# Performance work log

Hardware: AMD Instinct MI355X
Metric: run time of the kernel (lower is better)

## Reference

```python
import jax, jax.numpy as jnp
import numpy as np

HID = 512
POOL = 4096
NUM_OBJ = 151
NUM_REL = 51
K = 100
GROUPS = 8
EPS_GN = 1e-5


def _lrga(x, w, b):
    # LowRankAttention: x [N,D] -> [N,2K]
    tmp = jax.nn.relu(x @ w + b)            # [N,4K]
    u, v, z, t = tmp[:, :K], tmp[:, K:2*K], tmp[:, 2*K:3*K], tmp[:, 3*K:]
    # joint_normalize2: scalar 1 / (mean_n(U @ (V^T 1)) + eps)
    norm = u @ jnp.sum(v, axis=0)           # [N]
    d = 1.0 / (jnp.sum(norm) / x.shape[0] + 1e-6)
    res = u @ (v.T @ z)                     # [N,K], low-rank global attention
    return jax.nn.relu(jnp.concatenate((res * d, t), axis=1))


def _group_norm(x, gamma, beta):
    n, c = x.shape
    xg = x.reshape(n, GROUPS, c // GROUPS)
    mu = jnp.mean(xg, axis=-1, keepdims=True)
    var = jnp.var(xg, axis=-1, keepdims=True)
    xn = ((xg - mu) * jax.lax.rsqrt(var + EPS_GN)).reshape(n, c)
    return xn * gamma + beta


def setup_inputs() -> dict:
    key = jax.random.key(0)
    ks = jax.random.split(key, 24)
    n_obj, n_rel = 4096, 16384
    s = 0.02
    inp = {
        'edge_ctx': jax.random.normal(ks[0], (n_obj, HID), jnp.float32),
        'union_features': jax.random.normal(ks[1], (n_rel, POOL), jnp.float32),
        'rel_pair_idxs': jax.random.randint(ks[2], (n_rel, 2), 0, n_obj),
        'obj_preds': jax.random.randint(ks[3], (n_obj,), 0, NUM_OBJ),
        # parameters
        'w_post_emb': jax.random.normal(ks[4], (HID, 2 * HID), jnp.float32) * s,
        'b_post_emb': jnp.zeros((2 * HID,), jnp.float32),
        'w_post_cat': jax.random.normal(ks[5], (2 * HID, POOL), jnp.float32) * s,
        'b_post_cat': jnp.zeros((POOL,), jnp.float32),
        'w_attn1': jax.random.normal(ks[6], (POOL, 4 * K), jnp.float32) * s,
        'b_attn1': jnp.zeros((4 * K,), jnp.float32),
        'w_dr1': jax.random.normal(ks[7], (2 * K + POOL, POOL), jnp.float32) * s,
        'b_dr1': jnp.zeros((POOL,), jnp.float32),
        'gn_gamma': jnp.ones((POOL,), jnp.float32),
        'gn_beta': jnp.zeros((POOL,), jnp.float32),
        'w_attn2': jax.random.normal(ks[8], (POOL, 4 * K), jnp.float32) * s,
        'b_attn2': jnp.zeros((4 * K,), jnp.float32),
        'w_dr2': jax.random.normal(ks[9], (2 * K + POOL, POOL), jnp.float32) * s,
        'b_dr2': jnp.zeros((POOL,), jnp.float32),
        'w_rel': jax.random.normal(ks[10], (POOL, NUM_REL), jnp.float32) * s,
        'b_rel': jnp.zeros((NUM_REL,), jnp.float32),
        'w_ctx': jax.random.normal(ks[11], (2 * HID, NUM_REL), jnp.float32) * s,
        'b_ctx': jnp.zeros((NUM_REL,), jnp.float32),
        'freq_table': jax.random.normal(ks[12], (NUM_OBJ * NUM_OBJ, NUM_REL), jnp.float32) * s,
    }
    return inp


def reference(edge_ctx, union_features, rel_pair_idxs, obj_preds,
              w_post_emb, b_post_emb, w_post_cat, b_post_cat,
              w_attn1, b_attn1, w_dr1, b_dr1, gn_gamma, gn_beta,
              w_attn2, b_attn2, w_dr2, b_dr2,
              w_rel, b_rel, w_ctx, b_ctx, freq_table):
    # post_emb -> split into head/tail halves (view(N,2,H))
    edge_rep = edge_ctx @ w_post_emb + b_post_emb        # [N_obj, 2H]
    head_rep, tail_rep = edge_rep[:, :HID], edge_rep[:, HID:]
    # gather subject/object features per relation pair
    sub, obj = rel_pair_idxs[:, 0], rel_pair_idxs[:, 1]
    prod_rep = jnp.concatenate((head_rep[sub], tail_rep[obj]), axis=-1)  # [N_rel, 2H]
    pair_pred = obj_preds[rel_pair_idxs]                 # [N_rel, 2]
    ctx_gate = prod_rep @ w_post_cat + b_post_cat        # [N_rel, POOL]
    visual_rep = union_features * ctx_gate
    # LRGA block 1
    x_local = jax.nn.relu(visual_rep)                    # dropout = identity (eval)
    x_global = _lrga(union_features, w_attn1, b_attn1)   # [N_rel, 2K]
    x = jnp.concatenate((x_global, x_local), axis=1) @ w_dr1 + b_dr1
    x = _group_norm(jax.nn.relu(x), gn_gamma, gn_beta)
    # LRGA block 2
    x_local = jax.nn.relu(x)
    x_global = _lrga(x, w_attn2, b_attn2)
    visual_rep = jnp.concatenate((x_global, x_local), axis=1) @ w_dr2 + b_dr2
    # fused classification + frequency-bias lookup-add
    rel_dists = visual_rep @ w_rel + b_rel + prod_rep @ w_ctx + b_ctx
    freq = freq_table[pair_pred[:, 0] * NUM_OBJ + pair_pred[:, 1]]
    rel_dists = rel_dists + freq                         # dropout(0.3) = identity (eval)
    return rel_dists
```

## Files before the change

kernel.cpp:

```cpp
#include <hip/hip_runtime.h>

__device__ __forceinline__ short f2bf(float f) {
    unsigned u = __float_as_uint(f);
    unsigned r = (u + 0x7FFFu + ((u >> 16) & 1u)) >> 16;
    return (short)r;
}
__device__ __forceinline__ float bf2f(short s) {
    return __uint_as_float(((unsigned)(unsigned short)s) << 16);
}

typedef short bf16x8 __attribute__((ext_vector_type(8)));
typedef float f32x4  __attribute__((ext_vector_type(4)));

__device__ __forceinline__ void async16(const void* g, void* l) {
    __builtin_amdgcn_global_load_lds(
        (__attribute__((address_space(1))) unsigned int*)(void*)(g),
        (__attribute__((address_space(3))) unsigned int*)(l), 16, 0, 0);
}

template<int MODE>
__global__ __launch_bounds__(256)
void gemm128(const short* __restrict__ A, long lda,
             const short* __restrict__ B,
             const float* __restrict__ bias,
             void* __restrict__ outp, long ldo, int ooff, int nreal,
             const float* __restrict__ gate, short* __restrict__ gate_bf,
             const int* __restrict__ fidx, const float* __restrict__ freq,
             int K)
{
    __shared__ short As[128 * 64];
    __shared__ short Bs[128 * 64];
    const int t = threadIdx.x;
    const int lane = t & 63;
    const int w = t >> 6;
    const long bm = (long)blockIdx.y * 128;
    const long bn = (long)blockIdx.x * 128;

    f32x4 acc[4][4] = {};

    const short* Ab = A + bm * lda;
    const short* Bb = B + bn * (long)K;

    const int wm = (w & 1) * 64, wn = (w >> 1) * 64;
    const int mrow = lane & 15, khi = (lane >> 4) * 8;
    const int swz = mrow & 7;

    for (int k0 = 0; k0 < K; k0 += 64) {
        __syncthreads();
        #pragma unroll
        for (int i = 0; i < 4; ++i) {
            int idx = i * 256 + t;
            int r = idx >> 3, ch = (idx & 7) ^ (r & 7);
            async16(Ab + (long)r * lda + (k0 + ch * 8), &As[idx * 8]);
        }
        #pragma unroll
        for (int i = 0; i < 4; ++i) {
            int idx = i * 256 + t;
            int r = idx >> 3, ch = (idx & 7) ^ (r & 7);
            async16(Bb + (long)r * K + (k0 + ch * 8), &Bs[idx * 8]);
        }
        __syncthreads();

        #pragma unroll
        for (int kk = 0; kk < 64; kk += 32) {
            const int ch = (((kk + khi) >> 3) ^ swz) * 8;
            bf16x8 a[4], b[4];
            #pragma unroll
            for (int im = 0; im < 4; ++im)
                a[im] = *(const bf16x8*)&As[(wm + im * 16 + mrow) * 64 + ch];
            #pragma unroll
            for (int in = 0; in < 4; ++in)
                b[in] = *(const bf16x8*)&Bs[(wn + in * 16 + mrow) * 64 + ch];
            #pragma unroll
            for (int im = 0; im < 4; ++im)
                #pragma unroll
                for (int in = 0; in < 4; ++in)
                    acc[im][in] = __builtin_amdgcn_mfma_f32_16x16x32_bf16(
                        a[im], b[in], acc[im][in], 0, 0, 0);
        }
    }

    const int col = lane & 15, rb = (lane >> 4) * 4;
    #pragma unroll
    for (int in = 0; in < 4; ++in) {
        long n = bn + wn + in * 16 + col;
        if (n >= nreal) continue;
        float bv = bias[n];
        #pragma unroll
        for (int im = 0; im < 4; ++im) {
            #pragma unroll
            for (int r = 0; r < 4; ++r) {
                long m = bm + wm + im * 16 + rb + r;
                float v = acc[im][in][r] + bv;
                if (MODE == 1) v = fmaxf(v, 0.f);
                if (MODE == 2) {
                    float g = gate[m * 4096 + n];
                    gate_bf[m * 4096 + n] = f2bf(g);
                    v = fmaxf(v * g, 0.f);
                }
                if (MODE == 3) {
                    v += freq[(long)fidx[m] * 51 + n];
                    ((float*)outp)[m * 51 + n] = v;
                } else {
                    ((short*)outp)[m * ldo + ooff + n] = f2bf(v);
                }
            }
        }
    }
}

__global__ void cvt_bf16(const float* __restrict__ in, short* __restrict__ out, long n) {
    long i = (long)blockIdx.x * 256 + threadIdx.x;
    if (i < n) out[i] = f2bf(in[i]);
}

__global__ __launch_bounds__(256)
void transpose_pad(const float* __restrict__ in, int R, int C,
                   short* __restrict__ out, int Cp, int Rp)
{
    __shared__ float tile[32][33];
    int tx = threadIdx.x, ty = threadIdx.y;
    int c0 = blockIdx.x * 32, r0 = blockIdx.y * 32;
    #pragma unroll
    for (int j = 0; j < 32; j += 8) {
        int r = r0 + ty + j, c = c0 + tx;
        tile[ty + j][tx] = (r < R && c < C) ? in[(long)r * C + c] : 0.f;
    }
    __syncthreads();
    #pragma unroll
    for (int j = 0; j < 32; j += 8) {
        int oc = c0 + ty + j;
        int orr = r0 + tx;
        out[(long)oc * Rp + orr] = f2bf(tile[tx][ty + j]);
    }
}

__global__ void build_wf(const float* __restrict__ w_rel, const float* __restrict__ b_rel,
                         const float* __restrict__ w_ctx, const float* __restrict__ b_ctx,
                         short* __restrict__ wf, float* __restrict__ biasF)
{
    long i = (long)blockIdx.x * 256 + threadIdx.x;
    if (i < 64) biasF[i] = (i < 51) ? b_rel[i] + b_ctx[i] : 0.f;
    if (i >= 128L * 5120) return;
    int n = (int)(i / 5120), k = (int)(i % 5120);
    float v = 0.f;
    if (n < 51) v = (k < 4096) ? w_rel[(long)k * 51 + n] : w_ctx[(long)(k - 4096) * 51 + n];
    wf[i] = f2bf(v);
}

__global__ void gather_prod(const short* __restrict__ erep, const int* __restrict__ pairs,
                            const int* __restrict__ obj_preds,
                            short* __restrict__ vrcat, int* __restrict__ fidx)
{
    long i = blockIdx.x;
    int t = threadIdx.x;
    int s = pairs[2 * i], o = pairs[2 * i + 1];
    if (t == 0) fidx[i] = obj_preds[s] * 151 + obj_preds[o];
    int c = t * 4;
    long src = (long)(c < 512 ? s : o) * 1024 + c;
    *(uint2*)(vrcat + i * 5120 + 4096 + c) = *(const uint2*)(erep + src);
}

__global__ void colsum200(const short* __restrict__ tmp, float* __restrict__ colsum) {
    int t = threadIdx.x;
    if (t >= 200) return;
    const short* p = tmp + (long)blockIdx.x * 128 * 400 + t;
    float s = 0.f;
    for (int r = 0; r < 128; ++r) s += bf2f(p[(long)r * 400]);
    atomicAdd(&colsum[t], s);
}

__global__ void compute_d(const float* __restrict__ cs, float* __restrict__ dout) {
    int t = threadIdx.x;
    float v = cs[t] * cs[100 + t];
    if (t < 36) v += cs[64 + t] * cs[164 + t];
    #pragma unroll
    for (int m = 32; m >= 1; m >>= 1) v += __shfl_xor(v, m, 64);
    if (t == 0) dout[0] = 1.f / (v / 16384.f + 1e-6f);
}

__global__ __launch_bounds__(256)
void vtz_kern(const short* __restrict__ tmp, float* __restrict__ vtz) {
    __shared__ float vs[64 * 100];
    __shared__ float zs[64 * 100];
    int t = threadIdx.x;
    long r0 = (long)blockIdx.x * 64;
    for (int i = t; i < 64 * 200; i += 256) {
        int r = i / 200, c = i % 200;
        float val = bf2f(tmp[(r0 + r) * 400 + 100 + c]);
        if (c < 100) vs[r * 100 + c] = val; else zs[r * 100 + (c - 100)] = val;
    }
    __syncthreads();
    for (int e = t; e < 10000; e += 256) {
        int k = e / 100, l = e % 100;
        float s = 0.f;
        #pragma unroll 4
        for (int r = 0; r < 64; ++r) s += vs[r * 100 + k] * zs[r * 100 + l];
        atomicAdd(&vtz[e], s);
    }
}

__global__ __launch_bounds__(256)
void res_kern(const short* __restrict__ tmp, const float* __restrict__ vtz,
              const float* __restrict__ dptr, short* __restrict__ xcat)
{
    __shared__ float vt[10000];
    __shared__ float us[32 * 100];
    int t = threadIdx.x;
    long r0 = (long)blockIdx.x * 32;
    for (int i = t; i < 10000; i += 256) vt[i] = vtz[i];
    for (int i = t; i < 3200; i += 256) {
        int r = i / 100, c = i % 100;
        us[i] = bf2f(tmp[(r0 + r) * 400 + c]);
    }
    __syncthreads();
    float d = dptr[0];
    for (int e = t; e < 3200; e += 256) {
        int r = e / 100, c = e % 100;
        float s = 0.f;
        #pragma unroll 4
        for (int k = 0; k < 100; ++k) s += us[r * 100 + k] * vt[k * 100 + c];
        xcat[(r0 + r) * 4352 + c] = f2bf(fmaxf(s * d, 0.f));
    }
    for (int e = t; e < 3200; e += 256) {
        int r = e / 100, c = e % 100;
        xcat[(r0 + r) * 4352 + 100 + c] = tmp[(r0 + r) * 400 + 300 + c];
    }
    for (int e = t; e < 32 * 56; e += 256) {
        int r = e / 56, c = e % 56;
        xcat[(r0 + r) * 4352 + 4296 + c] = 0;
    }
}

__global__ __launch_bounds__(256)
void gn_kern(const short* __restrict__ y, const float* __restrict__ gamma,
             const float* __restrict__ beta,
             short* __restrict__ xgn, short* __restrict__ x2cat)
{
    long row = blockIdx.x;
    int t = threadIdx.x;
    const short* p = y + row * 4096 + t * 16;
    const uint4* q = (const uint4*)p;
    uint4 q0 = q[0], q1 = q[1];
    unsigned u[8] = {q0.x, q0.y, q0.z, q0.w, q1.x, q1.y, q1.z, q1.w};
    float v[16];
    #pragma unroll
    for (int i = 0; i < 8; ++i) {
        v[2 * i]     = __uint_as_float(u[i] << 16);
        v[2 * i + 1] = __uint_as_float(u[i] & 0xFFFF0000u);
    }
    float s1 = 0.f, s2 = 0.f;
    #pragma unroll
    for (int i = 0; i < 16; ++i) { s1 += v[i]; s2 += v[i] * v[i]; }
    #pragma unroll
    for (int m = 1; m < 32; m <<= 1) { s1 += __shfl_xor(s1, m, 32); s2 += __shfl_xor(s2, m, 32); }
    float mu = s1 * (1.f / 512.f);
    float var = fmaxf(s2 * (1.f / 512.f) - mu * mu, 0.f);
    float rs = rsqrtf(var + 1e-5f);
    #pragma unroll
    for (int i = 0; i < 16; ++i) {
        int c = t * 16 + i;
        float val = (v[i] - mu) * rs * gamma[c] + beta[c];
        xgn[row * 4096 + c] = f2bf(val);
        x2cat[row * 4352 + 200 + c] = f2bf(fmaxf(val, 0.f));
    }
}

extern "C" void kernel_launch(void* const* d_in, const int* in_sizes, int n_in,
                              void* d_out, int out_size, void* d_ws, size_t ws_size,
                              hipStream_t stream)
{
    (void)in_sizes; (void)n_in; (void)out_size; (void)ws_size;
    const float* edge_ctx   = (const float*)d_in[0];
    const float* unionf     = (const float*)d_in[1];
    const int*   pairs      = (const int*)d_in[2];
    const int*   obj_preds  = (const int*)d_in[3];
    const float* w_post_emb = (const float*)d_in[4];
    const float* b_post_emb = (const float*)d_in[5];
    const float* w_post_cat = (const float*)d_in[6];
    const float* b_post_cat = (const float*)d_in[7];
    const float* w_attn1    = (const float*)d_in[8];
    const float* b_attn1    = (const float*)d_in[9];
    const float* w_dr1      = (const float*)d_in[10];
    const float* b_dr1      = (const float*)d_in[11];
    const float* gamma      = (const float*)d_in[12];
    const float* beta       = (const float*)d_in[13];
    const float* w_attn2    = (const float*)d_in[14];
    const float* b_attn2    = (const float*)d_in[15];
    const float* w_dr2      = (const float*)d_in[16];
    const float* b_dr2      = (const float*)d_in[17];
    const float* w_rel      = (const float*)d_in[18];
    const float* b_rel      = (const float*)d_in[19];
    const float* w_ctx      = (const float*)d_in[20];
    const float* b_ctx      = (const float*)d_in[21];
    const float* freq       = (const float*)d_in[22];

    char* base = (char*)d_ws;
    size_t off = 0;
    auto alloc = [&](size_t b) -> void* {
        void* p = base + off; off += (b + 255) & ~(size_t)255; return p;
    };
    short* ec_bf  = (short*)alloc(4096L * 512 * 2);
    short* wTpe   = (short*)alloc(1024L * 512 * 2);
    short* erep   = (short*)alloc(4096L * 1024 * 2);
    short* vrcat  = (short*)alloc(16384L * 5120 * 2);
    int*   fidx   = (int*)  alloc(16384L * 4);
    short* ubf    = (short*)alloc(16384L * 4096 * 2);
    short* wTpc   = (short*)alloc(4096L * 1024 * 2);
    short* x1cat  = (short*)alloc(16384L * 4352 * 2);
    short* wTa1   = (short*)alloc(512L * 4096 * 2);
    short* wTa2   = (short*)alloc(512L * 4096 * 2);
    short* tmp    = (short*)alloc(16384L * 400 * 2);
    short* wTd1   = (short*)alloc(4096L * 4352 * 2);
    short* wTd2   = (short*)alloc(4096L * 4352 * 2);
    short* x2cat  = (short*)alloc(16384L * 4352 * 2);
    short* wF     = (short*)alloc(128L * 5120 * 2);
    float* biasF  = (float*)alloc(64 * 4);
    float* colsum = (float*)alloc(400 * 4);
    float* vtz    = (float*)alloc(100 * 100 * 4);
    float* dval   = (float*)alloc(4);

    dim3 tb(32, 8);
    cvt_bf16<<<(4096 * 512 + 255) / 256, 256, 0, stream>>>(edge_ctx, ec_bf, 4096L * 512);
    transpose_pad<<<dim3(1024 / 32, 512 / 32), tb, 0, stream>>>(w_post_emb, 512, 1024, wTpe, 1024, 512);
    transpose_pad<<<dim3(4096 / 32, 1024 / 32), tb, 0, stream>>>(w_post_cat, 1024, 4096, wTpc, 4096, 1024);
    transpose_pad<<<dim3(512 / 32, 4096 / 32), tb, 0, stream>>>(w_attn1, 4096, 400, wTa1, 512, 4096);
    transpose_pad<<<dim3(512 / 32, 4096 / 32), tb, 0, stream>>>(w_attn2, 4096, 400, wTa2, 512, 4096);
    transpose_pad<<<dim3(4096 / 32, 4352 / 32), tb, 0, stream>>>(w_dr1, 4296, 4096, wTd1, 4096, 4352);
    transpose_pad<<<dim3(4096 / 32, 4352 / 32), tb, 0, stream>>>(w_dr2, 4296, 4096, wTd2, 4096, 4352);
    build_wf<<<(128 * 5120 + 255) / 256, 256, 0, stream>>>(w_rel, b_rel, w_ctx, b_ctx, wF, biasF);

    gemm128<0><<<dim3(8, 32), 256, 0, stream>>>(ec_bf, 512, wTpe, b_post_emb,
        erep, 1024, 0, 1024, nullptr, nullptr, nullptr, nullptr, 512);
    gather_prod<<<16384, 256, 0, stream>>>(erep, pairs, obj_preds, vrcat, fidx);

    gemm128<2><<<dim3(32, 128), 256, 0, stream>>>(vrcat + 4096, 5120, wTpc, b_post_cat,
        x1cat, 4352, 200, 4096, unionf, ubf, nullptr, nullptr, 1024);

    gemm128<1><<<dim3(4, 128), 256, 0, stream>>>(ubf, 4096, wTa1, b_attn1,
        tmp, 400, 0, 400, nullptr, nullptr, nullptr, nullptr, 4096);
    hipMemsetAsync(colsum, 0, 400 * 4, stream);
    hipMemsetAsync(vtz, 0, 100 * 100 * 4, stream);
    colsum200<<<128, 256, 0, stream>>>(tmp, colsum);
    compute_d<<<1, 64, 0, stream>>>(colsum, dval);
    vtz_kern<<<256, 256, 0, stream>>>(tmp, vtz);
    res_kern<<<512, 256, 0, stream>>>(tmp, vtz, dval, x1cat);

    gemm128<1><<<dim3(32, 128), 256, 0, stream>>>(x1cat, 4352, wTd1, b_dr1,
        ubf, 4096, 0, 4096, nullptr, nullptr, nullptr, nullptr, 4352);
    gn_kern<<<16384, 256, 0, stream>>>(ubf, gamma, beta, x1cat, x2cat);

    gemm128<1><<<dim3(4, 128), 256, 0, stream>>>(x1cat, 4096, wTa2, b_attn2,
        tmp, 400, 0, 400, nullptr, nullptr, nullptr, nullptr, 4096);
    hipMemsetAsync(colsum, 0, 400 * 4, stream);
    hipMemsetAsync(vtz, 0, 100 * 100 * 4, stream);
    colsum200<<<128, 256, 0, stream>>>(tmp, colsum);
    compute_d<<<1, 64, 0, stream>>>(colsum, dval);
    vtz_kern<<<256, 256, 0, stream>>>(tmp, vtz);
    res_kern<<<512, 256, 0, stream>>>(tmp, vtz, dval, x2cat);

    gemm128<0><<<dim3(32, 128), 256, 0, stream>>>(x2cat, 4352, wTd2, b_dr2,
        vrcat, 5120, 0, 4096, nullptr, nullptr, nullptr, nullptr, 4352);
    gemm128<3><<<dim3(1, 128), 256, 0, stream>>>(vrcat, 5120, wF, biasF,
        d_out, 51, 0, 51, nullptr, nullptr, fidx, freq, 5120);
}
```

Before: 3.031 ms.

## Add 256x256 double-buffered MFMA GEMM with XCD-aware block remap for large GEMMs

Adds a new 512-thread GEMM kernel that computes 256x256 output tiles. It double-buffers 64-wide K slices in LDS with async global-to-LDS loads and interleaves the staging with MFMA quadrants, using explicit waitcnt/barrier scheduling and setprio. Block indices are remapped so that neighbouring tiles are spread across the eight XCDs. The three big 16384x4096 GEMMs switch to this kernel to raise data reuse per block and hide load latency. In exchange it uses 128 KB of LDS and many accumulator registers, which cuts occupancy, and the hand-placed synchronisation is fragile.

After: 2.720 ms. 1.11x faster.

```diff
diff --git a/kernel.cpp b/kernel.cpp
--- a/kernel.cpp
+++ b/kernel.cpp
@@ -17,6 +17,11 @@
         (__attribute__((address_space(1))) unsigned int*)(void*)(g),
         (__attribute__((address_space(3))) unsigned int*)(l), 16, 0, 0);
 }
+
+#define BAR()   __builtin_amdgcn_s_barrier()
+#define LGKM0() asm volatile("s_waitcnt lgkmcnt(0)" ::: "memory")
+#define VMW(n)  asm volatile("s_waitcnt vmcnt(" #n ")" ::: "memory")
+#define CLOB()  asm volatile("" ::: "memory")
 
 template<int MODE>
 __global__ __launch_bounds__(256)
@@ -104,6 +109,186 @@
                 } else {
                     ((short*)outp)[m * ldo + ooff + n] = f2bf(v);
                 }
+            }
+        }
+    }
+}
+
+template<int MH>
+__device__ __forceinline__ void loadAf(bf16x8 (&a)[4][2], const short* Asb,
+                                       int wrow, int fr, int kc0) {
+    #pragma unroll
+    for (int im = 0; im < 4; ++im) {
+        int r = wrow * 128 + MH * 64 + im * 16 + fr;
+        const short* rp = Asb + r * 64;
+        int s = r & 7;
+        a[im][0] = *(const bf16x8*)(rp + ((kc0    ) ^ s) * 8);
+        a[im][1] = *(const bf16x8*)(rp + ((kc0 + 4) ^ s) * 8);
+    }
+}
+template<int NH>
+__device__ __forceinline__ void loadBf(bf16x8 (&bb)[2][2], const short* Bsb,
+                                       int wcol, int fr, int kc0) {
+    #pragma unroll
+    for (int in = 0; in < 2; ++in) {
+        int r = wcol * 64 + NH * 32 + in * 16 + fr;
+        const short* rp = Bsb + r * 64;
+        int s = r & 7;
+        bb[in][0] = *(const bf16x8*)(rp + ((kc0    ) ^ s) * 8);
+        bb[in][1] = *(const bf16x8*)(rp + ((kc0 + 4) ^ s) * 8);
+    }
+}
+template<int MH, int NH>
+__device__ __forceinline__ void quadf(f32x4 (&acc)[8][4], const bf16x8 (&a)[4][2],
+                                      const bf16x8 (&bb)[2][2]) {
+    #pragma unroll
+    for (int ks = 0; ks < 2; ++ks)
+        #pragma unroll
+        for (int im = 0; im < 4; ++im)
+            #pragma unroll
+            for (int in = 0; in < 2; ++in)
+                acc[MH * 4 + im][NH * 2 + in] = __builtin_amdgcn_mfma_f32_16x16x32_bf16(
+                    a[im][ks], bb[in][ks], acc[MH * 4 + im][NH * 2 + in], 0, 0, 0);
+}
+
+template<int MODE>
+__global__ __launch_bounds__(512)
+void gemm256(const short* __restrict__ A, long lda,
+             const short* __restrict__ B,
+             const float* __restrict__ bias,
+             void* __restrict__ outp, long ldo, int ooff, int nreal,
+             const float* __restrict__ gate, short* __restrict__ gate_bf,
+             int K)
+{
+    __shared__ short As[2][256 * 64];
+    __shared__ short Bs[2][256 * 64];
+    const int t = threadIdx.x;
+    const int lane = t & 63;
+    const int w = t >> 6;
+    const int wrow = w >> 2, wcol = w & 3;
+
+    const int gx = gridDim.x;
+    int lin = blockIdx.y * gx + blockIdx.x;
+    int q8 = (gx * gridDim.y) >> 3;
+    int lin2 = (lin & 7) * q8 + (lin >> 3);
+    const long bm = (long)(lin2 / gx) * 256;
+    const long bn = (long)(lin2 % gx) * 256;
+
+    const short* Ab = A + bm * lda;
+    const short* Bb = B + bn * (long)K;
+
+    const int tq = t >> 3;
+    const int scz = (t & 7) ^ (tq & 7);
+    const long aoff = (long)tq * lda + scz * 8;
+    const int  brw  = (tq >> 5) * 64 + (tq & 31);
+    const long boff = (long)brw * K + scz * 8;
+    const int  blds = brw * 8 + (t & 7);
+
+    const int fr = lane & 15, kc0 = lane >> 4;
+
+    auto stgA = [&](int buf, int p, long tile) {
+        long k0 = tile << 6;
+        #pragma unroll
+        for (int j = 0; j < 2; ++j) {
+            int u = j * 128 + p * 64;
+            async16(Ab + (long)u * lda + k0 + aoff, &As[buf][u * 64 + t * 8]);
+        }
+    };
+    auto stgB = [&](int buf, int p, long tile) {
+        long k0 = tile << 6;
+        #pragma unroll
+        for (int j = 0; j < 2; ++j) {
+            int u = j * 128 + p * 32;
+            async16(Bb + (long)u * K + k0 + boff, &Bs[buf][u * 64 + blds * 8]);
+        }
+    };
+
+    f32x4 acc[8][4] = {};
+    bf16x8 a[4][2], b0[2][2], b1[2][2];
+
+    const int NT = K >> 6, NI = NT >> 1;
+
+    stgA(0, 0, 0); stgB(0, 0, 0); stgA(0, 1, 0); stgB(0, 1, 0);
+    stgA(1, 0, 1); stgB(1, 0, 1); stgA(1, 1, 1);
+    VMW(6);
+    BAR();
+
+    for (int it = 0; it < NI; ++it) {
+        const long T0 = 2 * it, T1 = 2 * it + 1;
+        const bool m0 = (T0 + 2 < NT), m1 = (T1 + 2 < NT);
+        const bool last = (it == NI - 1);
+        CLOB();
+        loadAf<0>(a, As[0], wrow, fr, kc0);
+        loadBf<0>(b0, Bs[0], wcol, fr, kc0);
+        stgB(1, 1, T1);
+        BAR(); LGKM0();
+        __builtin_amdgcn_s_setprio(1); quadf<0, 0>(acc, a, b0); __builtin_amdgcn_s_setprio(0);
+        BAR();
+        CLOB();
+        loadBf<1>(b1, Bs[0], wcol, fr, kc0);
+        if (m0) stgA(0, 0, T0 + 2);
+        BAR(); LGKM0();
+        __builtin_amdgcn_s_setprio(1); quadf<0, 1>(acc, a, b1); __builtin_amdgcn_s_setprio(0);
+        BAR();
+        CLOB();
+        loadAf<1>(a, As[0], wrow, fr, kc0);
+        if (m0) stgB(0, 0, T0 + 2);
+        BAR(); LGKM0();
+        __builtin_amdgcn_s_setprio(1); quadf<1, 0>(acc, a, b0); __builtin_amdgcn_s_setprio(0);
+        BAR();
+        CLOB();
+        if (m0) stgA(0, 1, T0 + 2);
+        if (last) { VMW(0); } else { VMW(6); }
+        BAR();
+        __builtin_amdgcn_s_setprio(1); quadf<1, 1>(acc, a, b1); __builtin_amdgcn_s_setprio(0);
+        BAR();
+        CLOB();
+        loadAf<0>(a, As[1], wrow, fr, kc0);
+        loadBf<0>(b0, Bs[1], wcol, fr, kc0);
+        if (m0) stgB(0, 1, T0 + 2);
+        BAR(); LGKM0();
+        __builtin_amdgcn_s_setprio(1); quadf<0, 0>(acc, a, b0); __builtin_amdgcn_s_setprio(0);
+        BAR();
+        CLOB();
+        loadBf<1>(b1, Bs[1], wcol, fr, kc0);
+        if (m1) stgA(1, 0, T1 + 2);
+        BAR(); LGKM0();
+        __builtin_amdgcn_s_setprio(1); quadf<0, 1>(acc, a, b1); __builtin_amdgcn_s_setprio(0);
+        BAR();
+        CLOB();
+        loadAf<1>(a, As[1], wrow, fr, kc0);
+        if (m1) stgB(1, 0, T1 + 2);
+        BAR(); LGKM0();
+        __builtin_amdgcn_s_setprio(1); quadf<1, 0>(acc, a, b0); __builtin_amdgcn_s_setprio(0);
+        BAR();
+        CLOB();
+        if (m1) stgA(1, 1, T1 + 2);
+        if (last) { VMW(0); } else { VMW(6); }
+        BAR();
+        __builtin_amdgcn_s_setprio(1); quadf<1, 1>(acc, a, b1); __builtin_amdgcn_s_setprio(0);
+        BAR();
+    }
+    VMW(0);
+
+    const int col = lane & 15, rb = (lane >> 4) * 4;
+    #pragma unroll
+    for (int in = 0; in < 4; ++in) {
+        long n = bn + wcol * 64 + in * 16 + col;
+        if (n >= nreal) continue;
+        float bv = bias[n];
+        #pragma unroll
+        for (int im = 0; im < 8; ++im) {
+            #pragma unroll
+            for (int r = 0; r < 4; ++r) {
+                long m = bm + wrow * 128 + im * 16 + rb + r;
+                float v = acc[im][in][r] + bv;
+                if (MODE == 1) v = fmaxf(v, 0.f);
+                if (MODE == 2) {
+                    float g = gate[m * 4096 + n];
+                    gate_bf[m * 4096 + n] = f2bf(g);
+                    v = fmaxf(v * g, 0.f);
+                }
+                ((short*)outp)[m * ldo + ooff + n] = f2bf(v);
             }
         }
     }
@@ -334,8 +519,8 @@
         erep, 1024, 0, 1024, nullptr, nullptr, nullptr, nullptr, 512);
     gather_prod<<<16384, 256, 0, stream>>>(erep, pairs, obj_preds, vrcat, fidx);
 
-    gemm128<2><<<dim3(32, 128), 256, 0, stream>>>(vrcat + 4096, 5120, wTpc, b_post_cat,
-        x1cat, 4352, 200, 4096, unionf, ubf, nullptr, nullptr, 1024);
+    gemm256<2><<<dim3(16, 64), 512, 0, stream>>>(vrcat + 4096, 5120, wTpc, b_post_cat,
+        x1cat, 4352, 200, 4096, unionf, ubf, 1024);
 
     gemm128<1><<<dim3(4, 128), 256, 0, stream>>>(ubf, 4096, wTa1, b_attn1,
         tmp, 400, 0, 400, nullptr, nullptr, nullptr, nullptr, 4096);
@@ -346,8 +531,8 @@
     vtz_kern<<<256, 256, 0, stream>>>(tmp, vtz);
     res_kern<<<512, 256, 0, stream>>>(tmp, vtz, dval, x1cat);
 
-    gemm128<1><<<dim3(32, 128), 256, 0, stream>>>(x1cat, 4352, wTd1, b_dr1,
-        ubf, 4096, 0, 4096, nullptr, nullptr, nullptr, nullptr, 4352);
+    gemm256<1><<<dim3(16, 64), 512, 0, stream>>>(x1cat, 4352, wTd1, b_dr1,
+        ubf, 4096, 0, 4096, nullptr, nullptr, 4352);
     gn_kern<<<16384, 256, 0, stream>>>(ubf, gamma, beta, x1cat, x2cat);
 
     gemm128<1><<<dim3(4, 128), 256, 0, stream>>>(x1cat, 4096, wTa2, b_attn2,
@@ -359,8 +544,8 @@
     vtz_kern<<<256, 256, 0, stream>>>(tmp, vtz);
     res_kern<<<512, 256, 0, stream>>>(tmp, vtz, dval, x2cat);
 
-    gemm128<0><<<dim3(32, 128), 256, 0, stream>>>(x2cat, 4352, wTd2, b_dr2,
-        vrcat, 5120, 0, 4096, nullptr, nullptr, nullptr, nullptr, 4352);
+    gemm256<0><<<dim3(16, 64), 512, 0, stream>>>(x2cat, 4352, wTd2, b_dr2,
+        vrcat, 5120, 0, 4096, nullptr, nullptr, 4352);
     gemm128<3><<<dim3(1, 128), 256, 0, stream>>>(vrcat, 5120, wF, biasF,
         d_out, 51, 0, 51, nullptr, nullptr, fidx, freq, 5120);
 }
```
